# Performance work log

Hardware: AMD Instinct MI355X
Metric: run time of the kernel (lower is better)

Reference implementation:

```python
import jax, jax.numpy as jnp
import numpy as np

HEADS = 16
HEAD_DIM = 128
HIDDEN = HEADS * HEAD_DIM  # 2048
B = 4
S = 2048  # max (padded) sequence length


def setup_inputs() -> dict:
    key = jax.random.key(0)
    k1, k2, k3 = jax.random.split(key, 3)
    x = jax.random.normal(k1, (B, S, HIDDEN), dtype=jnp.float32)
    W_qkv = jax.random.normal(k2, (HIDDEN, 3 * HIDDEN), dtype=jnp.float32) * 0.02
    b_qkv = jax.random.normal(k3, (3 * HIDDEN,), dtype=jnp.float32) * 0.02
    # jagged lengths mirroring the source's TOKENS // (i + 1) pattern
    lengths = jnp.array([S // (i + 1) for i in range(B)], dtype=jnp.int64)
    return {"x": x, "W_qkv": W_qkv, "b_qkv": b_qkv, "lengths": lengths}


def reference(x, W_qkv, b_qkv, lengths):
    # x: [B, S, HIDDEN] padded jagged batch; lengths: [B] valid token counts
    qkv = x @ W_qkv + b_qkv                       # [B, S, 3*HIDDEN]
    q, k, v = jnp.split(qkv, 3, axis=-1)          # each [B, S, HIDDEN]

    def to_heads(t):  # [B, S, HIDDEN] -> [B, H, S, D]
        return t.reshape(B, S, HEADS, HEAD_DIM).transpose(0, 2, 1, 3)

    q, k, v = to_heads(q), to_heads(k), to_heads(v)

    scale = 1.0 / jnp.sqrt(jnp.asarray(HEAD_DIM, dtype=q.dtype))
    scores = jnp.einsum('bhqd,bhkd->bhqk', q, k) * scale  # [B, H, S, S]

    valid = jnp.arange(S)[None, :] < lengths[:, None]     # [B, S]
    neg = jnp.asarray(-1e30, dtype=scores.dtype)
    scores = jnp.where(valid[:, None, None, :], scores, neg)

    attn = jax.nn.softmax(scores, axis=-1)                # [B, H, S, S]
    out = jnp.einsum('bhqk,bhkd->bhqd', attn, v)          # [B, H, S, D]
    # zero out padded query rows (they don't exist in the nested tensor)
    out = out * valid[:, None, :, None].astype(out.dtype)
    return out
```

## Files before the change

### kernel.cpp

```cpp
#include <hip/hip_runtime.h>
#include <stdint.h>

#define BATCH 4
#define SEQ   2048
#define NH    16
#define HD    128
#define HID   2048
#define N3    6144

typedef _Float16 f16;
typedef _Float16 f16x8 __attribute__((ext_vector_type(8)));
typedef _Float16 f16x4 __attribute__((ext_vector_type(4)));
typedef float    f32x4 __attribute__((ext_vector_type(4)));

#define QSCALE 0.1275313895f

__device__ __forceinline__ int get_len(const int* L, int b) {
  return (L[1] == 0) ? L[2 * b] : L[b];
}

__device__ __forceinline__ void async_copy16(void* lds_uniform, const void* gptr) {
  __builtin_amdgcn_global_load_lds(
      (const __attribute__((address_space(1))) void*)(uintptr_t)gptr,
      (__attribute__((address_space(3))) void*)(uint32_t)(uintptr_t)lds_uniform,
      16, 0, 0);
}

__global__ __launch_bounds__(256) void cvt_x(const float* __restrict__ x,
                                             f16* __restrict__ xh) {
  int idx = blockIdx.x * 256 + threadIdx.x;
  int m = idx >> 8;
  int g = idx & 255;
  int p = (g & ~3) | ((g ^ ((m >> 1) & 3)) & 3);
  const float* src = x + (size_t)m * HID + g * 8;
  f16x8 o;
#pragma unroll
  for (int j = 0; j < 8; ++j) o[j] = (f16)src[j];
  *(f16x8*)&xh[(size_t)m * HID + p * 8] = o;
}

__global__ __launch_bounds__(256) void cvt_w(const float* __restrict__ W,
                                             f16* __restrict__ Wt) {
  __shared__ float tile[64][65];
  const int n0 = blockIdx.x * 64;
  const int k0 = blockIdx.y * 64;
  const int tid = threadIdx.x;
#pragma unroll
  for (int i = 0; i < 4; ++i) {
    int id = tid + i * 256;
    int kr = id >> 4, nc = id & 15;
    f32x4 v = *(const f32x4*)&W[(size_t)(k0 + kr) * N3 + n0 + nc * 4];
#pragma unroll
    for (int j = 0; j < 4; ++j) tile[kr][nc * 4 + j] = v[j];
  }
  __syncthreads();
#pragma unroll
  for (int i = 0; i < 2; ++i) {
    int id = tid + i * 256;
    int nl = id >> 3;
    int kc = id & 7;
    f16x8 o;
#pragma unroll
    for (int j = 0; j < 8; ++j) o[j] = (f16)tile[kc * 8 + j][nl];
    int n = n0 + nl;
    int gk = (k0 >> 3) + kc;
    int p = (gk & ~3) | ((gk ^ ((n >> 1) & 3)) & 3);
    *(f16x8*)&Wt[(size_t)n * HID + p * 8] = o;
  }
}

__global__ __launch_bounds__(256, 3)
void qkv_gemm(const f16* __restrict__ xh, const f16* __restrict__ Wt,
              const float* __restrict__ bias, const int* __restrict__ lens,
              f16* __restrict__ Qh, f16* __restrict__ Kh, f16* __restrict__ Vt) {
  __shared__ f16 As[128 * 32];
  __shared__ f16 Bs[128 * 32];

  const int tid = threadIdx.x;
  const int wave = tid >> 6, lane = tid & 63;
  const int lr = lane & 15, quad = lane >> 4;
  const int nblk = blockIdx.x;
  const int mblk = blockIdx.y;
  const int m0 = mblk * 128;
  const int b = m0 >> 11;
  const int s0 = m0 & (SEQ - 1);
  const int len = get_len(lens, b);
  if (s0 >= len) return;
  const int n0 = nblk * 128;
  const int wr = (wave >> 1) * 64;
  const int wc = (wave & 1) * 64;

  f32x4 acc[4][4] = {};
  const char* xbase = (const char*)xh + (size_t)m0 * (HID * 2);
  const char* wbase = (const char*)Wt + (size_t)n0 * (HID * 2);

  for (int k0 = 0; k0 < HID; k0 += 32) {
    __syncthreads();
#pragma unroll
    for (int i = 0; i < 2; ++i) {
      int slot = wave * 2 + i;
      int row = slot * 16 + (lane >> 2);
      async_copy16(&As[slot * 512],
                   xbase + (size_t)row * (HID * 2) + k0 * 2 + (lane & 3) * 16);
      async_copy16(&Bs[slot * 512],
                   wbase + (size_t)row * (HID * 2) + k0 * 2 + (lane & 3) * 16);
    }
    __syncthreads();

    f16x8 a[4], bf[4];
#pragma unroll
    for (int mt = 0; mt < 4; ++mt) {
      int row = wr + mt * 16 + lr;
      int c = quad ^ ((row >> 1) & 3);
      a[mt] = *(const f16x8*)&As[row * 32 + c * 8];
    }
#pragma unroll
    for (int nt = 0; nt < 4; ++nt) {
      int row = wc + nt * 16 + lr;
      int c = quad ^ ((row >> 1) & 3);
      bf[nt] = *(const f16x8*)&Bs[row * 32 + c * 8];
    }
#pragma unroll
    for (int mt = 0; mt < 4; ++mt)
#pragma unroll
      for (int nt = 0; nt < 4; ++nt)
        acc[mt][nt] = __builtin_amdgcn_mfma_f32_16x16x32_f16(a[mt], bf[nt],
                                                             acc[mt][nt], 0, 0, 0);
  }

  const int t = nblk >> 4;
  const int h = nblk & 15;
  const size_t bhoff = (size_t)(b * NH + h);

  if (t == 0) {
    f16* qp = Qh + bhoff * (SEQ * HD);
#pragma unroll
    for (int nt = 0; nt < 4; ++nt) {
      int d = wc + nt * 16 + lr;
      float bv = bias[n0 + d];
#pragma unroll
      for (int mt = 0; mt < 4; ++mt) {
        int sb = s0 + wr + mt * 16 + quad * 4;
#pragma unroll
        for (int r = 0; r < 4; ++r)
          qp[(size_t)(sb + r) * HD + d] = (f16)((acc[mt][nt][r] + bv) * QSCALE);
      }
    }
  } else if (t == 1) {
    f16* kp = Kh + bhoff * (SEQ * HD);
#pragma unroll
    for (int nt = 0; nt < 4; ++nt) {
      int d = wc + nt * 16 + lr;
      float bv = bias[n0 + d];
#pragma unroll
      for (int mt = 0; mt < 4; ++mt) {
        int sb = s0 + wr + mt * 16 + quad * 4;
#pragma unroll
        for (int r = 0; r < 4; ++r) {
          int s = sb + r;
          int c = (d >> 3) ^ (s & 15);
          kp[(size_t)s * HD + c * 8 + (d & 7)] = (f16)(acc[mt][nt][r] + bv);
        }
      }
    }
  } else {
    f16* vp = Vt + bhoff * (HD * SEQ);
#pragma unroll
    for (int nt = 0; nt < 4; ++nt) {
      int d = wc + nt * 16 + lr;
      float bv = bias[n0 + d];
#pragma unroll
      for (int mt = 0; mt < 4; ++mt) {
        int sb = s0 + wr + mt * 16 + quad * 4;
        f16x4 pk;
#pragma unroll
        for (int r = 0; r < 4; ++r) pk[r] = (f16)(acc[mt][nt][r] + bv);
        int p = (sb >> 3) ^ (d & 7);
        *(f16x4*)&vp[(size_t)d * SEQ + p * 8 + (sb & 7)] = pk;
      }
    }
  }
}

__global__ __launch_bounds__(512, 4)
void attn(const f16* __restrict__ Qh, const f16* __restrict__ Kh,
          const f16* __restrict__ Vt, const int* __restrict__ lens,
          float* __restrict__ out) {
  __shared__ f16 Ks[64 * 128];
  __shared__ f16 Vs[128 * 64];
  __shared__ f16 Ps[128 * 72];

  const int tid = threadIdx.x, wave = tid >> 6, lane = tid & 63;
  const int lr = lane & 15, quad = lane >> 4;
  const int id = blockIdx.x;
  const int bhlo = id & 7;
  const int r3 = id >> 3;
  const int qt = r3 & 15;
  const int bh = ((r3 >> 4) << 3) | bhlo;
  const int b = bh >> 4, h = bh & 15;
  const int len = get_len(lens, b);
  const int q0 = qt * 128;
  const size_t bho = (size_t)(b * NH + h);
  float* obase = out + bho * (size_t)(SEQ * HD);

  if (q0 >= len) {
    f32x4 z = {0.f, 0.f, 0.f, 0.f};
#pragma unroll
    for (int i = 0; i < 8; ++i) {
      int idx = tid + i * 512;
      *(f32x4*)&obase[(size_t)q0 * HD + (size_t)idx * 4] = z;
    }
    return;
  }

  f16x8 qa[4];
  {
    const f16* qp = Qh + bho * (size_t)(SEQ * HD);
    int row = q0 + wave * 16 + lr;
#pragma unroll
    for (int ks = 0; ks < 4; ++ks)
      qa[ks] = *(const f16x8*)&qp[(size_t)row * HD + ks * 32 + quad * 8];
  }

  float mrow[4], lrow[4];
#pragma unroll
  for (int r = 0; r < 4; ++r) { mrow[r] = -3.0e38f; lrow[r] = 0.f; }
  f32x4 oacc[8] = {};

  const char* kpl = (const char*)(Kh + bho * (size_t)(SEQ * HD));
  const char* vpl = (const char*)(Vt + bho * (size_t)(HD * SEQ));

  const int nkt = (len + 63) >> 6;

  f16x8 kpre[2], vpre[2];
  const int kslot0 = wave * 2;
  const int kkey = (lane >> 4);
  const int kcol = (lane & 15);
  const int vdr = (lane >> 3);
  const int vcol = (lane & 7);

#pragma unroll
  for (int i = 0; i < 2; ++i) {
    int slot = kslot0 + i;
    kpre[i] = *(const f16x8*)(kpl + ((size_t)(slot * 4 + kkey) * HD + kcol * 8) * 2);
    vpre[i] = *(const f16x8*)(vpl + ((size_t)(slot * 8 + vdr) * SEQ + vcol * 8) * 2);
  }

  for (int kt = 0; kt < nkt; ++kt) {
    __syncthreads();
#pragma unroll
    for (int i = 0; i < 2; ++i) {
      int slot = kslot0 + i;
      *(f16x8*)&Ks[slot * 512 + lane * 8] = kpre[i];
      *(f16x8*)&Vs[slot * 512 + lane * 8] = vpre[i];
    }
    __syncthreads();
    if (kt + 1 < nkt) {
      size_t koff = (size_t)(kt + 1) * 64;
#pragma unroll
      for (int i = 0; i < 2; ++i) {
        int slot = kslot0 + i;
        kpre[i] = *(const f16x8*)(kpl + ((koff + slot * 4 + kkey) * HD + kcol * 8) * 2);
        vpre[i] = *(const f16x8*)(vpl + ((size_t)(slot * 8 + vdr) * SEQ + koff + vcol * 8) * 2);
      }
    }

    f32x4 sacc[4] = {};
#pragma unroll
    for (int ks = 0; ks < 4; ++ks) {
      f16x8 kb[4];
#pragma unroll
      for (int nt = 0; nt < 4; ++nt) {
        int key = nt * 16 + lr;
        int c = (ks * 4 + quad) ^ (key & 15);
        kb[nt] = *(const f16x8*)&Ks[key * 128 + c * 8];
      }
#pragma unroll
      for (int nt = 0; nt < 4; ++nt)
        sacc[nt] = __builtin_amdgcn_mfma_f32_16x16x32_f16(qa[ks], kb[nt],
                                                          sacc[nt], 0, 0, 0);
    }

    const int kbase = kt * 64;
    if (kbase + 64 > len) {
#pragma unroll
      for (int nt = 0; nt < 4; ++nt)
        if (kbase + nt * 16 + lr >= len)
#pragma unroll
          for (int r = 0; r < 4; ++r) sacc[nt][r] = -3.0e38f;
    }

#pragma unroll
    for (int r = 0; r < 4; ++r) {
      float mx = fmaxf(fmaxf(sacc[0][r], sacc[1][r]),
                       fmaxf(sacc[2][r], sacc[3][r]));
      mx = fmaxf(mx, __shfl_xor(mx, 1));
      mx = fmaxf(mx, __shfl_xor(mx, 2));
      mx = fmaxf(mx, __shfl_xor(mx, 4));
      mx = fmaxf(mx, __shfl_xor(mx, 8));
      float mnew = fmaxf(mrow[r], mx);
      float alpha = exp2f(mrow[r] - mnew);
      mrow[r] = mnew;
      float ls = 0.f;
#pragma unroll
      for (int nt = 0; nt < 4; ++nt) {
        float p = exp2f(sacc[nt][r] - mnew);
        sacc[nt][r] = p;
        ls += p;
      }
      lrow[r] = lrow[r] * alpha + ls;
#pragma unroll
      for (int nt = 0; nt < 8; ++nt) oacc[nt][r] *= alpha;
    }

#pragma unroll
    for (int nt = 0; nt < 4; ++nt)
#pragma unroll
      for (int r = 0; r < 4; ++r)
        Ps[(wave * 16 + quad * 4 + r) * 72 + nt * 16 + lr] = (f16)sacc[nt][r];

#pragma unroll
    for (int ks = 0; ks < 2; ++ks) {
      f16x8 pa = *(const f16x8*)&Ps[(wave * 16 + lr) * 72 + ks * 32 + quad * 8];
#pragma unroll
      for (int nt = 0; nt < 8; ++nt) {
        int d = nt * 16 + lr;
        int c = (ks * 4 + quad) ^ (d & 7);
        f16x8 vb = *(const f16x8*)&Vs[d * 64 + c * 8];
        oacc[nt] = __builtin_amdgcn_mfma_f32_16x16x32_f16(pa, vb, oacc[nt],
                                                          0, 0, 0);
      }
    }
  }

#pragma unroll
  for (int r = 0; r < 4; ++r) {
    float l = lrow[r];
    l += __shfl_xor(l, 1);
    l += __shfl_xor(l, 2);
    l += __shfl_xor(l, 4);
    l += __shfl_xor(l, 8);
    lrow[r] = 1.0f / l;
  }
  {
    int sb = q0 + wave * 16 + quad * 4;
#pragma unroll
    for (int nt = 0; nt < 8; ++nt) {
      int d = nt * 16 + lr;
#pragma unroll
      for (int r = 0; r < 4; ++r) {
        int s = sb + r;
        obase[(size_t)s * HD + d] =
            (s < len) ? oacc[nt][r] * lrow[r] : 0.0f;
      }
    }
  }
}

extern "C" void kernel_launch(void* const* d_in, const int* in_sizes, int n_in,
                              void* d_out, int out_size, void* d_ws, size_t ws_size,
                              hipStream_t stream) {
  const float* x = (const float*)d_in[0];
  const float* W = (const float*)d_in[1];
  const float* bias = (const float*)d_in[2];
  const int* lens = (const int*)d_in[3];
  float* out = (float*)d_out;

  char* ws = (char*)d_ws;
  size_t off = 0;
  f16* xh = (f16*)(ws + off); off += (size_t)BATCH * SEQ * HID * 2;
  f16* Wt = (f16*)(ws + off); off += (size_t)N3 * HID * 2;
  f16* Qh = (f16*)(ws + off); off += (size_t)BATCH * NH * SEQ * HD * 2;
  f16* Kh = (f16*)(ws + off); off += (size_t)BATCH * NH * SEQ * HD * 2;
  f16* Vt = (f16*)(ws + off); off += (size_t)BATCH * NH * SEQ * HD * 2;

  cvt_x<<<(BATCH * SEQ * HID / 8) / 256, 256, 0, stream>>>(x, xh);
  cvt_w<<<dim3(N3 / 64, HID / 64), 256, 0, stream>>>(W, Wt);
  qkv_gemm<<<dim3(48, 64), 256, 0, stream>>>(xh, Wt, bias, lens, Qh, Kh, Vt);
  attn<<<1024, 512, 0, stream>>>(Qh, Kh, Vt, lens, out);
}
```

Baseline: 387.4 us.

## Double GEMM K-tile to 64 with 8-chunk swizzle and fuse conversion kernels

The QKV GEMM now stages a 64-wide K slice per iteration instead of 32. This halves the number of barrier pairs and async-load rounds per output tile. The fp16 swizzle for x and W is widened from 4 to 8 chunks so the new 128-byte rows stay bank-conflict free. The two fp32-to-fp16 conversion kernels are merged into one launch, which removes one kernel launch. In exchange, LDS use doubles, which may reduce occupancy under the 3-blocks-per-CU launch bound.

```diff
diff --git a/kernel.cpp b/kernel.cpp
--- a/kernel.cpp
+++ b/kernel.cpp
@@ -26,46 +26,50 @@
       16, 0, 0);
 }
 
-__global__ __launch_bounds__(256) void cvt_x(const float* __restrict__ x,
-                                             f16* __restrict__ xh) {
-  int idx = blockIdx.x * 256 + threadIdx.x;
-  int m = idx >> 8;
-  int g = idx & 255;
-  int p = (g & ~3) | ((g ^ ((m >> 1) & 3)) & 3);
-  const float* src = x + (size_t)m * HID + g * 8;
-  f16x8 o;
-#pragma unroll
-  for (int j = 0; j < 8; ++j) o[j] = (f16)src[j];
-  *(f16x8*)&xh[(size_t)m * HID + p * 8] = o;
-}
-
-__global__ __launch_bounds__(256) void cvt_w(const float* __restrict__ W,
-                                             f16* __restrict__ Wt) {
+__global__ __launch_bounds__(256) void cvt_fused(const float* __restrict__ x,
+                                                 f16* __restrict__ xh,
+                                                 const float* __restrict__ W,
+                                                 f16* __restrict__ Wt) {
   __shared__ float tile[64][65];
-  const int n0 = blockIdx.x * 64;
-  const int k0 = blockIdx.y * 64;
-  const int tid = threadIdx.x;
-#pragma unroll
-  for (int i = 0; i < 4; ++i) {
-    int id = tid + i * 256;
-    int kr = id >> 4, nc = id & 15;
-    f32x4 v = *(const f32x4*)&W[(size_t)(k0 + kr) * N3 + n0 + nc * 4];
-#pragma unroll
-    for (int j = 0; j < 4; ++j) tile[kr][nc * 4 + j] = v[j];
-  }
-  __syncthreads();
-#pragma unroll
-  for (int i = 0; i < 2; ++i) {
-    int id = tid + i * 256;
-    int nl = id >> 3;
-    int kc = id & 7;
+  if (blockIdx.x < 8192) {
+    int idx = blockIdx.x * 256 + threadIdx.x;
+    int m = idx >> 8;
+    int g = idx & 255;
+    int f = ((m >> 1) & 3) | ((m & 1) << 2);
+    int p = (g & ~7) | ((g & 7) ^ f);
+    const float* src = x + (size_t)m * HID + g * 8;
     f16x8 o;
 #pragma unroll
-    for (int j = 0; j < 8; ++j) o[j] = (f16)tile[kc * 8 + j][nl];
-    int n = n0 + nl;
-    int gk = (k0 >> 3) + kc;
-    int p = (gk & ~3) | ((gk ^ ((n >> 1) & 3)) & 3);
-    *(f16x8*)&Wt[(size_t)n * HID + p * 8] = o;
+    for (int j = 0; j < 8; ++j) o[j] = (f16)src[j];
+    *(f16x8*)&xh[(size_t)m * HID + p * 8] = o;
+  } else {
+    int bid = blockIdx.x - 8192;
+    const int n0 = (bid % 96) * 64;
+    const int k0 = (bid / 96) * 64;
+    const int tid = threadIdx.x;
+#pragma unroll
+    for (int i = 0; i < 4; ++i) {
+      int id = tid + i * 256;
+      int kr = id >> 4, nc = id & 15;
+      f32x4 v = *(const f32x4*)&W[(size_t)(k0 + kr) * N3 + n0 + nc * 4];
+#pragma unroll
+      for (int j = 0; j < 4; ++j) tile[kr][nc * 4 + j] = v[j];
+    }
+    __syncthreads();
+#pragma unroll
+    for (int i = 0; i < 2; ++i) {
+      int id = tid + i * 256;
+      int nl = id >> 3;
+      int kc = id & 7;
+      f16x8 o;
+#pragma unroll
+      for (int j = 0; j < 8; ++j) o[j] = (f16)tile[kc * 8 + j][nl];
+      int n = n0 + nl;
+      int gk = (k0 >> 3) + kc;
+      int f = ((n >> 1) & 3) | ((n & 1) << 2);
+      int p = (gk & ~7) | (kc ^ f);
+      *(f16x8*)&Wt[(size_t)n * HID + p * 8] = o;
+    }
   }
 }
 
@@ -73,8 +77,8 @@
 void qkv_gemm(const f16* __restrict__ xh, const f16* __restrict__ Wt,
               const float* __restrict__ bias, const int* __restrict__ lens,
               f16* __restrict__ Qh, f16* __restrict__ Kh, f16* __restrict__ Vt) {
-  __shared__ f16 As[128 * 32];
-  __shared__ f16 Bs[128 * 32];
+  __shared__ f16 As[128 * 64];
+  __shared__ f16 Bs[128 * 64];
 
   const int tid = threadIdx.x;
   const int wave = tid >> 6, lane = tid & 63;
@@ -94,38 +98,41 @@
   const char* xbase = (const char*)xh + (size_t)m0 * (HID * 2);
   const char* wbase = (const char*)Wt + (size_t)n0 * (HID * 2);
 
-  for (int k0 = 0; k0 < HID; k0 += 32) {
-    __syncthreads();
-#pragma unroll
-    for (int i = 0; i < 2; ++i) {
-      int slot = wave * 2 + i;
-      int row = slot * 16 + (lane >> 2);
+  for (int k0 = 0; k0 < HID; k0 += 64) {
+    __syncthreads();
+#pragma unroll
+    for (int i = 0; i < 4; ++i) {
+      int slot = wave * 4 + i;
+      int row = slot * 8 + (lane >> 3);
       async_copy16(&As[slot * 512],
-                   xbase + (size_t)row * (HID * 2) + k0 * 2 + (lane & 3) * 16);
+                   xbase + (size_t)row * (HID * 2) + k0 * 2 + (lane & 7) * 16);
       async_copy16(&Bs[slot * 512],
-                   wbase + (size_t)row * (HID * 2) + k0 * 2 + (lane & 3) * 16);
-    }
-    __syncthreads();
-
-    f16x8 a[4], bf[4];
-#pragma unroll
-    for (int mt = 0; mt < 4; ++mt) {
-      int row = wr + mt * 16 + lr;
-      int c = quad ^ ((row >> 1) & 3);
-      a[mt] = *(const f16x8*)&As[row * 32 + c * 8];
-    }
-#pragma unroll
-    for (int nt = 0; nt < 4; ++nt) {
-      int row = wc + nt * 16 + lr;
-      int c = quad ^ ((row >> 1) & 3);
-      bf[nt] = *(const f16x8*)&Bs[row * 32 + c * 8];
-    }
-#pragma unroll
-    for (int mt = 0; mt < 4; ++mt)
-#pragma unroll
-      for (int nt = 0; nt < 4; ++nt)
-        acc[mt][nt] = __builtin_amdgcn_mfma_f32_16x16x32_f16(a[mt], bf[nt],
-                                                             acc[mt][nt], 0, 0, 0);
+                   wbase + (size_t)row * (HID * 2) + k0 * 2 + (lane & 7) * 16);
+    }
+    __syncthreads();
+
+#pragma unroll
+    for (int h = 0; h < 2; ++h) {
+      f16x8 a[4], bf[4];
+#pragma unroll
+      for (int mt = 0; mt < 4; ++mt) {
+        int row = wr + mt * 16 + lr;
+        int p = ((h ^ (row & 1)) << 2) | (quad ^ ((row >> 1) & 3));
+        a[mt] = *(const f16x8*)&As[row * 64 + p * 8];
+      }
+#pragma unroll
+      for (int nt = 0; nt < 4; ++nt) {
+        int row = wc + nt * 16 + lr;
+        int p = ((h ^ (row & 1)) << 2) | (quad ^ ((row >> 1) & 3));
+        bf[nt] = *(const f16x8*)&Bs[row * 64 + p * 8];
+      }
+#pragma unroll
+      for (int mt = 0; mt < 4; ++mt)
+#pragma unroll
+        for (int nt = 0; nt < 4; ++nt)
+          acc[mt][nt] = __builtin_amdgcn_mfma_f32_16x16x32_f16(a[mt], bf[nt],
+                                                               acc[mt][nt], 0, 0, 0);
+    }
   }
 
   const int t = nblk >> 4;
@@ -374,8 +381,7 @@
   f16* Kh = (f16*)(ws + off); off += (size_t)BATCH * NH * SEQ * HD * 2;
   f16* Vt = (f16*)(ws + off); off += (size_t)BATCH * NH * SEQ * HD * 2;
 
-  cvt_x<<<(BATCH * SEQ * HID / 8) / 256, 256, 0, stream>>>(x, xh);
-  cvt_w<<<dim3(N3 / 64, HID / 64), 256, 0, stream>>>(W, Wt);
+  cvt_fused<<<8192 + 3072, 256, 0, stream>>>(x, xh, W, Wt);
   qkv_gemm<<<dim3(48, 64), 256, 0, stream>>>(xh, Wt, bias, lens, Qh, Kh, Vt);
   attn<<<1024, 512, 0, stream>>>(Qh, Kh, Vt, lens, out);
 }
```

Result: no change. 379.9 us (-2.0%).
